# Performance work log

Measured on AMD Instinct MI355X. Metric: run time of the kernel, lower is better.

The kernel has to match this reference:

```python
import jax, jax.numpy as jnp
import numpy as np

B, S, H = 2, 2048, 1024
N, DK = 16, 64          # heads, key/value dim (N*DK == H)
DF = 4096               # FFN hidden
SCALE = 1.0 / float(DK) ** 0.5
EPS = 1e-5


def _layer_norm(x, g, b):
    mu = jnp.mean(x, axis=-1, keepdims=True)
    var = jnp.var(x, axis=-1, keepdims=True)
    return (x - mu) * jax.lax.rsqrt(var + EPS) * g + b


def setup_inputs() -> dict:
    key = jax.random.key(0)
    ks = jax.random.split(key, 12)
    s = 0.02
    return {
        "x": jax.random.normal(ks[0], (B, S, H), dtype=jnp.float32),
        "Wq": jax.random.normal(ks[1], (N * DK, H), dtype=jnp.float32) * s,
        "bq": jnp.zeros((N * DK,), jnp.float32),
        "Wk": jax.random.normal(ks[2], (N * DK, H), dtype=jnp.float32) * s,
        "bk": jnp.zeros((N * DK,), jnp.float32),
        "Wv": jax.random.normal(ks[3], (N * DK, H), dtype=jnp.float32) * s,
        "bv": jnp.zeros((N * DK,), jnp.float32),
        "Wo": jax.random.normal(ks[4], (H, N * DK), dtype=jnp.float32) * s,
        "bo": jnp.zeros((H,), jnp.float32),
        "W1": jax.random.normal(ks[5], (DF, H), dtype=jnp.float32) * s,
        "b1": jnp.zeros((DF,), jnp.float32),
        "W2": jax.random.normal(ks[6], (H, DF), dtype=jnp.float32) * s,
        "b2": jnp.zeros((H,), jnp.float32),
        "ln1_g": jnp.ones((H,), jnp.float32),
        "ln1_b": jnp.zeros((H,), jnp.float32),
        "ln2_g": jnp.ones((H,), jnp.float32),
        "ln2_b": jnp.zeros((H,), jnp.float32),
    }


def _mha(x, Wq, bq, Wk, bk, Wv, bv, Wo, bo):
    b = x.shape[0]
    q = (x @ Wq.T + bq).reshape(b, -1, N, DK)  # [B,T,N,DK]
    k = (x @ Wk.T + bk).reshape(b, -1, N, DK)
    v = (x @ Wv.T + bv).reshape(b, -1, N, DK)
    # naive full-score attention, faithful to torch einsum layout
    scores = jnp.einsum('btnd,bsnd->tsbn', q, k) * SCALE  # [T,S,B,N]
    p = jax.nn.softmax(scores, axis=1)                    # softmax over S (dim=1)
    attn = jnp.einsum('tsbn,bsnd->btnd', p, v)            # [B,T,N,DK]
    attn = attn.reshape(b, attn.shape[1], -1)             # [B,T,N*DK]
    return attn @ Wo.T + bo


def reference(x, Wq, bq, Wk, bk, Wv, bv, Wo, bo, W1, b1, W2, b2,
              ln1_g, ln1_b, ln2_g, ln2_b):
    # post-LN encoder layer: x = LN(x + MHA(x)); x = LN(x + FFN(x))
    h = _layer_norm(x + _mha(x, Wq, bq, Wk, bk, Wv, bv, Wo, bo), ln1_g, ln1_b)
    ff = jax.nn.relu(h @ W1.T + b1) @ W2.T + b2
    return _layer_norm(h + ff, ln2_g, ln2_b)
```

## Files before the change

### kernel.cpp

```cpp
#include <hip/hip_runtime.h>
#include <stdint.h>


typedef unsigned short u16;
typedef __bf16 bf16x8 __attribute__((ext_vector_type(8)));
typedef float  f32x4  __attribute__((ext_vector_type(4)));

__device__ __forceinline__ u16 f2bf(float f) {
    unsigned int u = __float_as_uint(f);
    u += 0x7FFFu + ((u >> 16) & 1u);
    return (u16)(u >> 16);
}

__device__ __forceinline__ float bf2f(u16 v) {
    return __uint_as_float((unsigned)v << 16);
}

__device__ __forceinline__ unsigned pack_bf16_hi(float lo, float hi) {
#if __has_builtin(__builtin_amdgcn_perm)
    return __builtin_amdgcn_perm(__float_as_uint(hi), __float_as_uint(lo), 0x07060302u);
#else
    return (__float_as_uint(lo) >> 16) | (__float_as_uint(hi) & 0xFFFF0000u);
#endif
}

__device__ __forceinline__ void async_load16(const u16* g, u16* l) {
    __builtin_amdgcn_global_load_lds(
        (__attribute__((address_space(1))) void*)g,
        (__attribute__((address_space(3))) void*)l, 16, 0, 0);
}

struct CvtArgs {
    const float* src[7];
    u16*         dst[7];
    int          n[7];
};

__global__ __launch_bounds__(256) void k_cvt_all(CvtArgs a) {
    const int seg = blockIdx.y;
    const int i = (blockIdx.x * 256 + threadIdx.x) * 8;
    if (i >= a.n[seg]) return;
    const float* in = a.src[seg];
    u16* out = a.dst[seg];
    float4 x = *(const float4*)(in + i);
    float4 y = *(const float4*)(in + i + 4);
    uint4 o;
    o.x = (unsigned)f2bf(x.x) | ((unsigned)f2bf(x.y) << 16);
    o.y = (unsigned)f2bf(x.z) | ((unsigned)f2bf(x.w) << 16);
    o.z = (unsigned)f2bf(y.x) | ((unsigned)f2bf(y.y) << 16);
    o.w = (unsigned)f2bf(y.z) | ((unsigned)f2bf(y.w) << 16);
    *(uint4*)(out + i) = o;
}

__global__ __launch_bounds__(256) void k_concat3(const float* __restrict__ a,
                                                 const float* __restrict__ b,
                                                 const float* __restrict__ c,
                                                 float* __restrict__ out) {
    int i = blockIdx.x * 256 + threadIdx.x;
    if (i >= 3072) return;
    out[i] = (i < 1024) ? a[i] : (i < 2048 ? b[i - 1024] : c[i - 2048]);
}

template<int OUT_BF16, int RELU>
__global__ __launch_bounds__(256, 4) void k_gemm_bt(
    const u16* __restrict__ A, const u16* __restrict__ Bw,
    const float* __restrict__ bias, void* __restrict__ Y,
    int M, int N, int K)
{
    __shared__ u16 As[128 * 32];
    __shared__ u16 Bs[128 * 32];
    const int tid  = threadIdx.x;
    const int wave = tid >> 6, lane = tid & 63;
    const int lm = lane & 15, lq = lane >> 4;
    const int m0 = blockIdx.x * 128, n0 = blockIdx.y * 128;
    const int wr = (wave >> 1) * 64, wc = (wave & 1) * 64;

    const int ksz = K / gridDim.z;
    const int ks  = blockIdx.z * ksz, ke = ks + ksz;

    const size_t arow = (size_t)(m0 + (lane >> 2)) * K + (lane & 3) * 8;
    const size_t brow = (size_t)(n0 + (lane >> 2)) * K + (lane & 3) * 8;
    const int c0 = wave * 2, c1 = wave * 2 + 1;

    f32x4 acc[4][4];
#pragma unroll
    for (int i = 0; i < 4; i++)
#pragma unroll
        for (int j = 0; j < 4; j++) acc[i][j] = (f32x4){0.f, 0.f, 0.f, 0.f};

    for (int k0 = ks; k0 < ke; k0 += 32) {
        __syncthreads();
        async_load16(A  + arow + (size_t)(c0 * 16) * K + k0, As + c0 * 512);
        async_load16(A  + arow + (size_t)(c1 * 16) * K + k0, As + c1 * 512);
        async_load16(Bw + brow + (size_t)(c0 * 16) * K + k0, Bs + c0 * 512);
        async_load16(Bw + brow + (size_t)(c1 * 16) * K + k0, Bs + c1 * 512);
        __syncthreads();

        bf16x8 af[4], bf[4];
#pragma unroll
        for (int i = 0; i < 4; i++)
            af[i] = *(const bf16x8*)(As + (wr + i * 16 + lm) * 32 + lq * 8);
#pragma unroll
        for (int j = 0; j < 4; j++)
            bf[j] = *(const bf16x8*)(Bs + (wc + j * 16 + lm) * 32 + lq * 8);
#pragma unroll
        for (int i = 0; i < 4; i++)
#pragma unroll
            for (int j = 0; j < 4; j++)
                acc[i][j] = __builtin_amdgcn_mfma_f32_16x16x32_bf16(af[i], bf[j], acc[i][j], 0, 0, 0);
    }

    const float bsc = (blockIdx.z == 0) ? 1.f : 0.f;
    const size_t zoff = (size_t)blockIdx.z * M * N;
#pragma unroll
    for (int i = 0; i < 4; i++) {
        const int mg = m0 + wr + i * 16 + lq * 4;
#pragma unroll
        for (int j = 0; j < 4; j++) {
            const int ng = n0 + wc + j * 16 + lm;
            const float bv = bias[ng] * bsc;
#pragma unroll
            for (int r = 0; r < 4; r++) {
                float v = acc[i][j][r] + bv;
                if (RELU) v = fmaxf(v, 0.f);
                if (OUT_BF16) ((u16*)Y)[zoff + (size_t)(mg + r) * N + ng] = f2bf(v);
                else          ((float*)Y)[zoff + (size_t)(mg + r) * N + ng] = v;
            }
        }
    }
}

__global__ __launch_bounds__(256) void k_transpose_v(const u16* __restrict__ qkv,
                                                     u16* __restrict__ vt) {
    __shared__ u16 T[64 * 72];
    const int tid = threadIdx.x;
    const int t0 = blockIdx.x * 64;
    const int bn = blockIdx.y;
    const int b = bn >> 4, n = bn & 15;
    {
        const int r = tid >> 2, c = (tid & 3) * 16;
        const u16* src = qkv + (size_t)(b * 2048 + t0 + r) * 3072 + 2048 + n * 64 + c;
        *(uint4*)&T[r * 72 + c]     = *(const uint4*)(src);
        *(uint4*)&T[r * 72 + c + 8] = *(const uint4*)(src + 8);
    }
    __syncthreads();
    {
        const int d = tid >> 2, c = (tid & 3) * 16;
        union { u16 h[16]; uint4 v[2]; } tmp;
#pragma unroll
        for (int j = 0; j < 16; j++) {
            const int w = c + j;
            const int k = ((w & 3) << 4) + (w >> 2);
            tmp.h[j] = T[k * 72 + d];
        }
        u16* dst = vt + (size_t)(bn * 64 + d) * 2048 + t0 + c;
        *(uint4*)(dst)     = tmp.v[0];
        *(uint4*)(dst + 8) = tmp.v[1];
    }
}

__global__ __launch_bounds__(256, 2) void k_flash(const u16* __restrict__ qkv,
                                                  const u16* __restrict__ vt,
                                                  u16* __restrict__ attn) {
    __shared__ u16 Ks[64 * 72];
    __shared__ u16 Vs[64 * 72];
    __shared__ u16 Ps[4 * 32 * 72];
    const int tid = threadIdx.x, wave = tid >> 6, lane = tid & 63;
    const int lm = lane & 15, lq = lane >> 4;
    const int b = blockIdx.z, n = blockIdx.y, qt0 = blockIdx.x * 128;

    bf16x8 qf[2][2];
#pragma unroll
    for (int mh = 0; mh < 2; mh++) {
        const u16* qp = qkv + (size_t)(b * 2048 + qt0 + wave * 32 + mh * 16 + lm) * 3072
                        + n * 64 + lq * 8;
        const bf16x8 q0r = *(const bf16x8*)(qp);
        const bf16x8 q1r = *(const bf16x8*)(qp + 32);
#pragma unroll
        for (int j = 0; j < 8; j++) {
            qf[mh][0][j] = (__bf16)((float)q0r[j] * 0.18033688f);
            qf[mh][1][j] = (__bf16)((float)q1r[j] * 0.18033688f);
        }
    }

    float lsum[2][4];
    f32x4 oacc[2][4];
#pragma unroll
    for (int mh = 0; mh < 2; mh++)
#pragma unroll
        for (int r = 0; r < 4; r++) { lsum[mh][r] = 0.f; }
#pragma unroll
    for (int mh = 0; mh < 2; mh++)
#pragma unroll
        for (int dt = 0; dt < 4; dt++) oacc[mh][dt] = (f32x4){0.f, 0.f, 0.f, 0.f};

    const int sr = tid >> 2, sc = (tid & 3) * 16;
    const u16* kg = qkv + (size_t)(b * 2048 + sr) * 3072 + 1024 + n * 64 + sc;
    const u16* vg = vt + (size_t)((b * 16 + n) * 64 + sr) * 2048 + sc;
    u16* PsW = Ps + wave * 32 * 72;

    uint4 kr0 = *(const uint4*)(kg);
    uint4 kr1 = *(const uint4*)(kg + 8);
    uint4 vr0 = *(const uint4*)(vg);
    uint4 vr1 = *(const uint4*)(vg + 8);

    for (int kt = 0; kt < 2048; kt += 64) {
        __syncthreads();
        *(uint4*)&Ks[sr * 72 + sc]     = kr0;
        *(uint4*)&Ks[sr * 72 + sc + 8] = kr1;
        *(uint4*)&Vs[sr * 72 + sc]     = vr0;
        *(uint4*)&Vs[sr * 72 + sc + 8] = vr1;
        __syncthreads();

        if (kt + 64 < 2048) {
            kr0 = *(const uint4*)(kg + (size_t)(kt + 64) * 3072);
            kr1 = *(const uint4*)(kg + (size_t)(kt + 64) * 3072 + 8);
            vr0 = *(const uint4*)(vg + kt + 64);
            vr1 = *(const uint4*)(vg + kt + 64 + 8);
        }

        f32x4 sf[2][4];
#pragma unroll
        for (int nt = 0; nt < 4; nt++) {
            const bf16x8 kf0 = *(const bf16x8*)(Ks + (nt * 16 + lm) * 72 + lq * 8);
            const bf16x8 kf1 = *(const bf16x8*)(Ks + (nt * 16 + lm) * 72 + lq * 8 + 32);
#pragma unroll
            for (int mh = 0; mh < 2; mh++) {
                f32x4 z = (f32x4){0.f, 0.f, 0.f, 0.f};
                z = __builtin_amdgcn_mfma_f32_16x16x32_bf16(qf[mh][0], kf0, z, 0, 0, 0);
                z = __builtin_amdgcn_mfma_f32_16x16x32_bf16(qf[mh][1], kf1, z, 0, 0, 0);
                sf[mh][nt] = z;
            }
        }

#pragma unroll
        for (int mh = 0; mh < 2; mh++)
#pragma unroll
            for (int r = 0; r < 4; r++) {
                const float p0 = __builtin_amdgcn_exp2f(sf[mh][0][r]);
                const float p1 = __builtin_amdgcn_exp2f(sf[mh][1][r]);
                const float p2 = __builtin_amdgcn_exp2f(sf[mh][2][r]);
                const float p3 = __builtin_amdgcn_exp2f(sf[mh][3][r]);
                lsum[mh][r] += (p0 + p1) + (p2 + p3);
                uint2 w;
                w.x = pack_bf16_hi(p0, p1);
                w.y = pack_bf16_hi(p2, p3);
                *(uint2*)&PsW[(mh * 16 + lq * 4 + r) * 72 + lm * 4] = w;
            }

#pragma unroll
        for (int s2 = 0; s2 < 2; s2++) {
            bf16x8 pf[2];
#pragma unroll
            for (int mh = 0; mh < 2; mh++)
                pf[mh] = *(const bf16x8*)(PsW + (mh * 16 + lm) * 72 + s2 * 32 + lq * 8);
#pragma unroll
            for (int dt = 0; dt < 4; dt++) {
                const bf16x8 vf = *(const bf16x8*)(Vs + (dt * 16 + lm) * 72 + s2 * 32 + lq * 8);
#pragma unroll
                for (int mh = 0; mh < 2; mh++)
                    oacc[mh][dt] = __builtin_amdgcn_mfma_f32_16x16x32_bf16(pf[mh], vf, oacc[mh][dt], 0, 0, 0);
            }
        }
    }

#pragma unroll
    for (int mh = 0; mh < 2; mh++)
#pragma unroll
        for (int r = 0; r < 4; r++) {
#pragma unroll
            for (int off = 8; off >= 1; off >>= 1)
                lsum[mh][r] += __shfl_xor(lsum[mh][r], off, 16);
            lsum[mh][r] = 1.f / lsum[mh][r];
        }
#pragma unroll
    for (int mh = 0; mh < 2; mh++)
#pragma unroll
        for (int dt = 0; dt < 4; dt++)
#pragma unroll
            for (int r = 0; r < 4; r++) {
                const float o = oacc[mh][dt][r] * lsum[mh][r];
                attn[(size_t)(b * 2048 + qt0 + wave * 32 + mh * 16 + lq * 4 + r) * 1024
                     + n * 64 + dt * 16 + lm] = f2bf(o);
            }
}

template<int WRITE_BF16>
__global__ __launch_bounds__(256) void k_ln_p4(const float* __restrict__ a,
                                               const u16* __restrict__ pb,
                                               const float* __restrict__ g,
                                               const float* __restrict__ be,
                                               float* __restrict__ outf,
                                               u16* __restrict__ outb) {
    const int row = blockIdx.x, tid = threadIdx.x;
    const size_t base = (size_t)row * 1024 + tid * 4;
    const float4 av = *(const float4*)(a + base);
    float x0 = av.x, x1 = av.y, x2 = av.z, x3 = av.w;
#pragma unroll
    for (int z = 0; z < 4; z++) {
        const uint2 w = *(const uint2*)(pb + (size_t)z * 4096 * 1024 + base);
        x0 += __uint_as_float(w.x << 16);
        x1 += __uint_as_float(w.x & 0xFFFF0000u);
        x2 += __uint_as_float(w.y << 16);
        x3 += __uint_as_float(w.y & 0xFFFF0000u);
    }
    float s1 = x0 + x1 + x2 + x3;
    float s2 = x0 * x0 + x1 * x1 + x2 * x2 + x3 * x3;
#pragma unroll
    for (int off = 32; off >= 1; off >>= 1) {
        s1 += __shfl_down(s1, off);
        s2 += __shfl_down(s2, off);
    }
    __shared__ float red[8];
    __shared__ float stats[2];
    const int wave = tid >> 6, lane = tid & 63;
    if (lane == 0) { red[wave] = s1; red[4 + wave] = s2; }
    __syncthreads();
    if (tid == 0) {
        const float t1 = red[0] + red[1] + red[2] + red[3];
        const float t2 = red[4] + red[5] + red[6] + red[7];
        const float mean = t1 * (1.f / 1024.f);
        const float var = t2 * (1.f / 1024.f) - mean * mean;
        stats[0] = mean;
        stats[1] = rsqrtf(var + 1e-5f);
    }
    __syncthreads();
    const float mean = stats[0], rstd = stats[1];
    const int c = tid * 4;
    const float4 gv = *(const float4*)(g + c);
    const float4 bev = *(const float4*)(be + c);
    float4 y;
    y.x = (x0 - mean) * rstd * gv.x + bev.x;
    y.y = (x1 - mean) * rstd * gv.y + bev.y;
    y.z = (x2 - mean) * rstd * gv.z + bev.z;
    y.w = (x3 - mean) * rstd * gv.w + bev.w;
    *(float4*)(outf + base) = y;
    if (WRITE_BF16) {
        uint2 o;
        o.x = (unsigned)f2bf(y.x) | ((unsigned)f2bf(y.y) << 16);
        o.y = (unsigned)f2bf(y.z) | ((unsigned)f2bf(y.w) << 16);
        *(uint2*)(outb + base) = o;
    }
}

extern "C" void kernel_launch(void* const* d_in, const int* in_sizes, int n_in,
                              void* d_out, int out_size, void* d_ws, size_t ws_size,
                              hipStream_t stream) {
    const float* x   = (const float*)d_in[0];
    const float* Wq  = (const float*)d_in[1];
    const float* bq  = (const float*)d_in[2];
    const float* Wk  = (const float*)d_in[3];
    const float* bk  = (const float*)d_in[4];
    const float* Wv  = (const float*)d_in[5];
    const float* bv  = (const float*)d_in[6];
    const float* Wo  = (const float*)d_in[7];
    const float* bo  = (const float*)d_in[8];
    const float* W1  = (const float*)d_in[9];
    const float* b1  = (const float*)d_in[10];
    const float* W2  = (const float*)d_in[11];
    const float* b2  = (const float*)d_in[12];
    const float* g1  = (const float*)d_in[13];
    const float* be1 = (const float*)d_in[14];
    const float* g2  = (const float*)d_in[15];
    const float* be2 = (const float*)d_in[16];

    char* ws = (char*)d_ws;
    const size_t MB = 1024 * 1024;
    u16*   wqkv = (u16*)(ws + 0);
    u16*   wo_b = (u16*)(ws + 6 * MB);
    u16*   w1_b = (u16*)(ws + 8 * MB);
    u16*   w2_b = (u16*)(ws + 16 * MB);
    float* bqkv = (float*)(ws + 24 * MB);
    u16*   xb   = (u16*)(ws + 25 * MB);
    u16*   qkv  = (u16*)(ws + 33 * MB);
    u16*   vt   = (u16*)(ws + 57 * MB);
    u16*   attn = (u16*)(ws + 65 * MB);
    u16*   op4  = (u16*)(ws + 33 * MB);
    float* h    = (float*)(ws + 65 * MB);
    u16*   hb   = (u16*)(ws + 81 * MB);
    u16*   ff1  = (u16*)(ws + 33 * MB);
    u16*   fp4  = (u16*)(ws + 81 * MB);

    CvtArgs ca;
    ca.src[0] = x;  ca.dst[0] = xb;                  ca.n[0] = 4096 * 1024;
    ca.src[1] = Wq; ca.dst[1] = wqkv;                ca.n[1] = 1024 * 1024;
    ca.src[2] = Wk; ca.dst[2] = wqkv + 1024 * 1024;  ca.n[2] = 1024 * 1024;
    ca.src[3] = Wv; ca.dst[3] = wqkv + 2 * 1024 * 1024; ca.n[3] = 1024 * 1024;
    ca.src[4] = Wo; ca.dst[4] = wo_b;                ca.n[4] = 1024 * 1024;
    ca.src[5] = W1; ca.dst[5] = w1_b;                ca.n[5] = 4096 * 1024;
    ca.src[6] = W2; ca.dst[6] = w2_b;                ca.n[6] = 4096 * 1024;
    k_cvt_all<<<dim3(2048, 7), 256, 0, stream>>>(ca);
    k_concat3<<<12, 256, 0, stream>>>(bq, bk, bv, bqkv);

    k_gemm_bt<1, 0><<<dim3(32, 24), 256, 0, stream>>>(
        xb, wqkv, bqkv, qkv, 4096, 3072, 1024);

    k_transpose_v<<<dim3(32, 32), 256, 0, stream>>>(qkv, vt);

    k_flash<<<dim3(16, 16, 2), 256, 0, stream>>>(qkv, vt, attn);

    k_gemm_bt<1, 0><<<dim3(32, 8, 4), 256, 0, stream>>>(
        attn, wo_b, bo, op4, 4096, 1024, 1024);

    k_ln_p4<1><<<4096, 256, 0, stream>>>(x, op4, g1, be1, h, hb);

    k_gemm_bt<1, 1><<<dim3(32, 32), 256, 0, stream>>>(
        hb, w1_b, b1, ff1, 4096, 4096, 1024);

    k_gemm_bt<1, 0><<<dim3(32, 8, 4), 256, 0, stream>>>(
        ff1, w2_b, b2, fp4, 4096, 1024, 4096);

    k_ln_p4<0><<<4096, 256, 0, stream>>>(h, fp4, g2, be2, (float*)d_out, nullptr);
}
```

Before: 342.9 us.

## Split flash attention key range across two wave groups and merge partials

New measurement: 344.2 us. About the same (+0.4%).

```diff
diff --git a/kernel.cpp b/kernel.cpp
--- a/kernel.cpp
+++ b/kernel.cpp
@@ -10,10 +10,6 @@
     unsigned int u = __float_as_uint(f);
     u += 0x7FFFu + ((u >> 16) & 1u);
     return (u16)(u >> 16);
-}
-
-__device__ __forceinline__ float bf2f(u16 v) {
-    return __uint_as_float((unsigned)v << 16);
 }
 
 __device__ __forceinline__ unsigned pack_bf16_hi(float lo, float hi) {
@@ -159,20 +155,23 @@
     }
 }
 
-__global__ __launch_bounds__(256, 2) void k_flash(const u16* __restrict__ qkv,
+__global__ __launch_bounds__(512, 4) void k_flash(const u16* __restrict__ qkv,
                                                   const u16* __restrict__ vt,
                                                   u16* __restrict__ attn) {
-    __shared__ u16 Ks[64 * 72];
-    __shared__ u16 Vs[64 * 72];
-    __shared__ u16 Ps[4 * 32 * 72];
+    __shared__ u16 KV[4 * 64 * 72];
+    __shared__ u16 Ps[8 * 32 * 72];
     const int tid = threadIdx.x, wave = tid >> 6, lane = tid & 63;
+    const int h = wave >> 2, w4 = wave & 3;
     const int lm = lane & 15, lq = lane >> 4;
     const int b = blockIdx.z, n = blockIdx.y, qt0 = blockIdx.x * 128;
 
+    u16* KsH = KV + (h * 2 + 0) * 64 * 72;
+    u16* VsH = KV + (h * 2 + 1) * 64 * 72;
+
     bf16x8 qf[2][2];
 #pragma unroll
     for (int mh = 0; mh < 2; mh++) {
-        const u16* qp = qkv + (size_t)(b * 2048 + qt0 + wave * 32 + mh * 16 + lm) * 3072
+        const u16* qp = qkv + (size_t)(b * 2048 + qt0 + w4 * 32 + mh * 16 + lm) * 3072
                         + n * 64 + lq * 8;
         const bf16x8 q0r = *(const bf16x8*)(qp);
         const bf16x8 q1r = *(const bf16x8*)(qp + 32);
@@ -188,15 +187,18 @@
 #pragma unroll
     for (int mh = 0; mh < 2; mh++)
 #pragma unroll
-        for (int r = 0; r < 4; r++) { lsum[mh][r] = 0.f; }
+        for (int r = 0; r < 4; r++) lsum[mh][r] = 0.f;
 #pragma unroll
     for (int mh = 0; mh < 2; mh++)
 #pragma unroll
         for (int dt = 0; dt < 4; dt++) oacc[mh][dt] = (f32x4){0.f, 0.f, 0.f, 0.f};
 
-    const int sr = tid >> 2, sc = (tid & 3) * 16;
-    const u16* kg = qkv + (size_t)(b * 2048 + sr) * 3072 + 1024 + n * 64 + sc;
-    const u16* vg = vt + (size_t)((b * 16 + n) * 64 + sr) * 2048 + sc;
+    const int g = tid >> 8, ht = tid & 255;
+    const int sr = ht >> 2, sc = (ht & 3) * 16;
+    u16* KsG = KV + (g * 2 + 0) * 64 * 72;
+    u16* VsG = KV + (g * 2 + 1) * 64 * 72;
+    const u16* kg = qkv + (size_t)(b * 2048 + g * 1024 + sr) * 3072 + 1024 + n * 64 + sc;
+    const u16* vg = vt + (size_t)((b * 16 + n) * 64 + sr) * 2048 + g * 1024 + sc;
     u16* PsW = Ps + wave * 32 * 72;
 
     uint4 kr0 = *(const uint4*)(kg);
@@ -204,15 +206,15 @@
     uint4 vr0 = *(const uint4*)(vg);
     uint4 vr1 = *(const uint4*)(vg + 8);
 
-    for (int kt = 0; kt < 2048; kt += 64) {
-        __syncthreads();
-        *(uint4*)&Ks[sr * 72 + sc]     = kr0;
-        *(uint4*)&Ks[sr * 72 + sc + 8] = kr1;
-        *(uint4*)&Vs[sr * 72 + sc]     = vr0;
-        *(uint4*)&Vs[sr * 72 + sc + 8] = vr1;
-        __syncthreads();
-
-        if (kt + 64 < 2048) {
+    for (int kt = 0; kt < 1024; kt += 64) {
+        __syncthreads();
+        *(uint4*)&KsG[sr * 72 + sc]     = kr0;
+        *(uint4*)&KsG[sr * 72 + sc + 8] = kr1;
+        *(uint4*)&VsG[sr * 72 + sc]     = vr0;
+        *(uint4*)&VsG[sr * 72 + sc + 8] = vr1;
+        __syncthreads();
+
+        if (kt + 64 < 1024) {
             kr0 = *(const uint4*)(kg + (size_t)(kt + 64) * 3072);
             kr1 = *(const uint4*)(kg + (size_t)(kt + 64) * 3072 + 8);
             vr0 = *(const uint4*)(vg + kt + 64);
@@ -222,8 +224,8 @@
         f32x4 sf[2][4];
 #pragma unroll
         for (int nt = 0; nt < 4; nt++) {
-            const bf16x8 kf0 = *(const bf16x8*)(Ks + (nt * 16 + lm) * 72 + lq * 8);
-            const bf16x8 kf1 = *(const bf16x8*)(Ks + (nt * 16 + lm) * 72 + lq * 8 + 32);
+            const bf16x8 kf0 = *(const bf16x8*)(KsH + (nt * 16 + lm) * 72 + lq * 8);
+            const bf16x8 kf1 = *(const bf16x8*)(KsH + (nt * 16 + lm) * 72 + lq * 8 + 32);
 #pragma unroll
             for (int mh = 0; mh < 2; mh++) {
                 f32x4 z = (f32x4){0.f, 0.f, 0.f, 0.f};
@@ -256,7 +258,7 @@
                 pf[mh] = *(const bf16x8*)(PsW + (mh * 16 + lm) * 72 + s2 * 32 + lq * 8);
 #pragma unroll
             for (int dt = 0; dt < 4; dt++) {
-                const bf16x8 vf = *(const bf16x8*)(Vs + (dt * 16 + lm) * 72 + s2 * 32 + lq * 8);
+                const bf16x8 vf = *(const bf16x8*)(VsH + (dt * 16 + lm) * 72 + s2 * 32 + lq * 8);
 #pragma unroll
                 for (int mh = 0; mh < 2; mh++)
                     oacc[mh][dt] = __builtin_amdgcn_mfma_f32_16x16x32_bf16(pf[mh], vf, oacc[mh][dt], 0, 0, 0);
@@ -271,18 +273,38 @@
 #pragma unroll
             for (int off = 8; off >= 1; off >>= 1)
                 lsum[mh][r] += __shfl_xor(lsum[mh][r], off, 16);
-            lsum[mh][r] = 1.f / lsum[mh][r];
-        }
-#pragma unroll
-    for (int mh = 0; mh < 2; mh++)
-#pragma unroll
-        for (int dt = 0; dt < 4; dt++)
-#pragma unroll
-            for (int r = 0; r < 4; r++) {
-                const float o = oacc[mh][dt][r] * lsum[mh][r];
-                attn[(size_t)(b * 2048 + qt0 + wave * 32 + mh * 16 + lq * 4 + r) * 1024
-                     + n * 64 + dt * 16 + lm] = f2bf(o);
-            }
+        }
+
+    float* mbuf = (float*)KV;
+    __syncthreads();
+#pragma unroll
+    for (int mh = 0; mh < 2; mh++) {
+        const int base = (w4 * 64 + lane) * 20;
+        if (h == 1) {
+#pragma unroll
+            for (int dt = 0; dt < 4; dt++)
+#pragma unroll
+                for (int r = 0; r < 4; r++) mbuf[base + dt * 4 + r] = oacc[mh][dt][r];
+#pragma unroll
+            for (int r = 0; r < 4; r++) mbuf[base + 16 + r] = lsum[mh][r];
+        }
+        __syncthreads();
+        if (h == 0) {
+            float inv[4];
+#pragma unroll
+            for (int r = 0; r < 4; r++)
+                inv[r] = 1.f / (lsum[mh][r] + mbuf[base + 16 + r]);
+#pragma unroll
+            for (int dt = 0; dt < 4; dt++)
+#pragma unroll
+                for (int r = 0; r < 4; r++) {
+                    const float o = (oacc[mh][dt][r] + mbuf[base + dt * 4 + r]) * inv[r];
+                    attn[(size_t)(b * 2048 + qt0 + w4 * 32 + mh * 16 + lq * 4 + r) * 1024
+                         + n * 64 + dt * 16 + lm] = f2bf(o);
+                }
+        }
+        __syncthreads();
+    }
 }
 
 template<int WRITE_BF16>
@@ -397,7 +419,7 @@
 
     k_transpose_v<<<dim3(32, 32), 256, 0, stream>>>(qkv, vt);
 
-    k_flash<<<dim3(16, 16, 2), 256, 0, stream>>>(qkv, vt, attn);
+    k_flash<<<dim3(16, 16, 2), 512, 0, stream>>>(qkv, vt, attn);
 
     k_gemm_bt<1, 0><<<dim3(32, 8, 4), 256, 0, stream>>>(
         attn, wo_b, bo, op4, 4096, 1024, 1024);
```
